# Kernel tuning notes

Measured on AMD Instinct MI355X. Metric: run time of the kernel, lower is better.

## Reference

```python
import jax, jax.numpy as jnp
import numpy as np

K = 3  # kernel_size
P = K // 2


def setup_inputs() -> dict:
    key = jax.random.key(0)
    k1, k2 = jax.random.split(key)
    x = jax.random.normal(k1, (8, 64, 256, 256), dtype=jnp.float32)
    alpha = jnp.full((1, 64, 1, 1), 0.1, dtype=jnp.float32)
    return {"x": x, "alpha": alpha}


def reference(x, alpha):
    # Equivalent to F.unfold(x, K, padding=P) -> abs-diff from center -> sum over K*K -> residual.
    b, c, h, w = x.shape
    xp = jnp.pad(x, ((0, 0), (0, 0), (P, P), (P, P)))  # zero padding, same as F.unfold
    diff_sum = jnp.zeros_like(x)
    for di in range(K):
        for dj in range(K):
            neighbor = xp[:, :, di:di + h, dj:dj + w]
            diff_sum = diff_sum + jnp.abs(x - neighbor)
    return x + alpha * diff_sum
```

## Files before the change

kernel.cpp:

```cpp
#include <hip/hip_runtime.h>


constexpr int H = 256;
constexpr int W = 256;
constexpr int C = 64;

__global__ __launch_bounds__(256) void adc_kernel(
    const float* __restrict__ x,
    const float* __restrict__ alpha,
    float* __restrict__ out)
{
    const int lane = threadIdx.x & 63;
    const int wave = threadIdx.x >> 6;
    const long slab = (long)blockIdx.x;
    const long img  = slab >> 4;
    const int  s16  = (int)(slab & 15);
    const int  y0   = s16 * 16 + wave * 4;
    const int  c    = (int)(img & (C - 1));

    const float  a    = alpha[c];
    const float* imgp = x   + img * (long)(H * W);
    float*       outp = out + img * (long)(H * W);
    const int    w0   = lane * 4;

    float v[6][6];
#pragma unroll
    for (int r = 0; r < 6; ++r) {
        const int yy = y0 + r - 1;
        float4 ctr = make_float4(0.f, 0.f, 0.f, 0.f);
        if (yy >= 0 && yy < H)
            ctr = *(const float4*)(imgp + (long)yy * W + w0);
        v[r][1] = ctr.x; v[r][2] = ctr.y; v[r][3] = ctr.z; v[r][4] = ctr.w;
        const float left  = __shfl_up(ctr.w, 1);
        const float right = __shfl_down(ctr.x, 1);
        v[r][0] = (lane == 0)  ? 0.f : left;
        v[r][5] = (lane == 63) ? 0.f : right;
    }

#pragma unroll
    for (int o = 0; o < 4; ++o) {
        float4 res;
        float* rp = &res.x;
#pragma unroll
        for (int j = 0; j < 4; ++j) {
            const float xc = v[o + 1][j + 1];
            float s = 0.f;
#pragma unroll
            for (int r = 0; r < 3; ++r)
#pragma unroll
                for (int d = 0; d < 3; ++d)
                    s += fabsf(xc - v[o + r][j + d]);
            rp[j] = fmaf(a, s, xc);
        }
        *(float4*)(outp + (long)(y0 + o) * W + w0) = res;
    }
}

extern "C" void kernel_launch(void* const* d_in, const int* in_sizes, int n_in,
                              void* d_out, int out_size, void* d_ws, size_t ws_size,
                              hipStream_t stream)
{
    const float* x     = (const float*)d_in[0];
    const float* alpha = (const float*)d_in[1];
    float*       out   = (float*)d_out;

    const int grid = 8 * C * (H / 16);
    adc_kernel<<<grid, 256, 0, stream>>>(x, alpha, out);
}
```

Before: 235.1 us.

## Stage slab rows in LDS via direct global-to-LDS loads, remap blocks per XCD

Each block now loads its 18-row halo slab straight into shared memory with global_load_lds and a zero-padded stride, instead of having every wave load six rows with shuffles. Adjacent waves no longer re-read the same halo rows from global memory. Stencil rows are then read from LDS in a rolling three-row window. Block indices are remapped so that all slabs of an image run on the same XCD, and outputs use nontemporal stores. In exchange the kernel adds a barrier and LDS traffic, and the global_load_lds path depends on the lane-to-address layout being correct.

```diff
diff --git a/kernel.cpp b/kernel.cpp
--- a/kernel.cpp
+++ b/kernel.cpp
@@ -1,58 +1,107 @@
 #include <hip/hip_runtime.h>
+#include <stdint.h>
 
+
+typedef float f32x4 __attribute__((ext_vector_type(4)));
 
 constexpr int H = 256;
 constexpr int W = 256;
 constexpr int C = 64;
+constexpr int SLAB = 16;
+constexpr int NR   = SLAB + 2;
+constexpr int RSTR = 264;
+
+typedef const uint32_t __attribute__((address_space(1)))* gas_t;
+typedef uint32_t __attribute__((address_space(3)))* las_t;
 
 __global__ __launch_bounds__(256) void adc_kernel(
     const float* __restrict__ x,
     const float* __restrict__ alpha,
     float* __restrict__ out)
 {
-    const int lane = threadIdx.x & 63;
-    const int wave = threadIdx.x >> 6;
-    const long slab = (long)blockIdx.x;
-    const long img  = slab >> 4;
-    const int  s16  = (int)(slab & 15);
-    const int  y0   = s16 * 16 + wave * 4;
-    const int  c    = (int)(img & (C - 1));
+    __shared__ float lds[NR * RSTR];
 
-    const float  a    = alpha[c];
-    const float* imgp = x   + img * (long)(H * W);
-    float*       outp = out + img * (long)(H * W);
-    const int    w0   = lane * 4;
+    const int tid  = threadIdx.x;
+    const int lane = tid & 63;
+    const int wave = tid >> 6;
 
-    float v[6][6];
-#pragma unroll
-    for (int r = 0; r < 6; ++r) {
-        const int yy = y0 + r - 1;
-        float4 ctr = make_float4(0.f, 0.f, 0.f, 0.f);
-        if (yy >= 0 && yy < H)
-            ctr = *(const float4*)(imgp + (long)yy * W + w0);
-        v[r][1] = ctr.x; v[r][2] = ctr.y; v[r][3] = ctr.z; v[r][4] = ctr.w;
-        const float left  = __shfl_up(ctr.w, 1);
-        const float right = __shfl_down(ctr.x, 1);
-        v[r][0] = (lane == 0)  ? 0.f : left;
-        v[r][5] = (lane == 63) ? 0.f : right;
+    const int n     = blockIdx.x;
+    const int xcd   = n & 7;
+    const int local = n >> 3;
+    const int img   = ((local >> 4) << 3) + xcd;
+    const int slab  = local & 15;
+    const int y0    = slab * SLAB;
+
+    const float a = alpha[img & (C - 1)];
+    const float* imgp = x   + (long)img * (H * W);
+    float*       outp = out + (long)img * (H * W);
+
+    if (tid < NR) {
+        *(f32x4*)&lds[tid * RSTR] = (f32x4){0.f, 0.f, 0.f, 0.f};
+        lds[tid * RSTR + 260] = 0.f;
     }
 
 #pragma unroll
+    for (int r = wave; r < NR; r += 4) {
+        const int g = y0 + r - 1;
+        if (g >= 0 && g < H) {
+            const float* gsrc = imgp + (long)g * W + lane * 4;
+            __builtin_amdgcn_global_load_lds((gas_t)gsrc,
+                                             (las_t)&lds[r * RSTR + 4],
+                                             16, 0, 0);
+        } else {
+            *(f32x4*)&lds[r * RSTR + 4 + lane * 4] =
+                (f32x4){0.f, 0.f, 0.f, 0.f};
+        }
+    }
+    __syncthreads();
+
+    const int r0    = wave * 4 + 1;
+    const int cbase = 4 + lane * 4;
+
+    f32x4 eq[3];
+    float eL[3], eR[3];
+#pragma unroll
+    for (int k = 0; k < 2; ++k) {
+        const int rr = r0 - 1 + k;
+        eq[k] = *(const f32x4*)&lds[rr * RSTR + cbase];
+        eL[k] = lds[rr * RSTR + cbase - 1];
+        eR[k] = lds[rr * RSTR + cbase + 4];
+    }
+
+    float* orow0 = outp + (long)(y0 + wave * 4) * W + lane * 4;
+
+#pragma unroll
     for (int o = 0; o < 4; ++o) {
-        float4 res;
-        float* rp = &res.x;
+        const int s = (o + 2) % 3, t = o % 3, m = (o + 1) % 3;
+        const int rr = r0 + o + 1;
+        eq[s] = *(const f32x4*)&lds[rr * RSTR + cbase];
+        eL[s] = lds[rr * RSTR + cbase - 1];
+        eR[s] = lds[rr * RSTR + cbase + 4];
+
+        float e[3][6];
+#pragma unroll
+        for (int k = 0; k < 3; ++k) {
+            const int kk = (k == 0) ? t : ((k == 1) ? m : s);
+            e[k][0] = eL[kk];
+            e[k][1] = eq[kk].x; e[k][2] = eq[kk].y;
+            e[k][3] = eq[kk].z; e[k][4] = eq[kk].w;
+            e[k][5] = eR[kk];
+        }
+
+        f32x4 res;
 #pragma unroll
         for (int j = 0; j < 4; ++j) {
-            const float xc = v[o + 1][j + 1];
-            float s = 0.f;
+            const float xc = e[1][j + 1];
+            float sacc = 0.f;
 #pragma unroll
-            for (int r = 0; r < 3; ++r)
+            for (int r2 = 0; r2 < 3; ++r2)
 #pragma unroll
                 for (int d = 0; d < 3; ++d)
-                    s += fabsf(xc - v[o + r][j + d]);
-            rp[j] = fmaf(a, s, xc);
+                    sacc += fabsf(xc - e[r2][j + d]);
+            res[j] = fmaf(a, sacc, xc);
         }
-        *(float4*)(outp + (long)(y0 + o) * W + w0) = res;
+        __builtin_nontemporal_store(res, (f32x4*)(orow0 + o * W));
     }
 }
 
@@ -64,6 +113,6 @@
     const float* alpha = (const float*)d_in[1];
     float*       out   = (float*)d_out;
 
-    const int grid = 8 * C * (H / 16);
+    const int grid = 8 * C * (H / SLAB);
     adc_kernel<<<grid, 256, 0, stream>>>(x, alpha, out);
 }
```

After: 228.1 us. 3.0% less time.

## Stream rows through per-wave LDS ring with async global-to-LDS loads

Applied to the files above, without the earlier changes.

Each wave now processes 16 rows instead of 4, streaming input rows through an 8-slot LDS ring filled by global_load_lds. Explicit vmcnt waits keep several loads in flight, and the three-row window is rotated in registers. This cuts halo re-reads from 6/4 to 18/16 and overlaps loads with compute. It also remaps blocks so each image's slabs stay on one XCD and uses nontemporal stores, at the cost of more LDS per block and fragile manual waitcnt tuning.

```diff
diff --git a/kernel.cpp b/kernel.cpp
--- a/kernel.cpp
+++ b/kernel.cpp
@@ -1,59 +1,102 @@
 #include <hip/hip_runtime.h>
+#include <stdint.h>
 
 
-constexpr int H = 256;
-constexpr int W = 256;
-constexpr int C = 64;
+typedef float f32x4 __attribute__((ext_vector_type(4)));
+
+constexpr int H = 256, W = 256, C = 64;
+constexpr int RSTR = 256;
+
+typedef const uint32_t __attribute__((address_space(1)))* gas_t;
+typedef uint32_t __attribute__((address_space(3)))* las_t;
+
+#define WAITV(n) do { asm volatile("s_waitcnt vmcnt(" #n ")" ::: "memory"); \
+                      __builtin_amdgcn_sched_barrier(0); } while (0)
 
 __global__ __launch_bounds__(256) void adc_kernel(
     const float* __restrict__ x,
     const float* __restrict__ alpha,
     float* __restrict__ out)
 {
-    const int lane = threadIdx.x & 63;
-    const int wave = threadIdx.x >> 6;
-    const long slab = (long)blockIdx.x;
-    const long img  = slab >> 4;
-    const int  s16  = (int)(slab & 15);
-    const int  y0   = s16 * 16 + wave * 4;
-    const int  c    = (int)(img & (C - 1));
+    __shared__ float lds[4 * 8 * RSTR];
 
-    const float  a    = alpha[c];
-    const float* imgp = x   + img * (long)(H * W);
-    float*       outp = out + img * (long)(H * W);
-    const int    w0   = lane * 4;
+    const int tid  = threadIdx.x, lane = tid & 63, wave = tid >> 6;
+    const int n    = blockIdx.x, xcd = n & 7, local = n >> 3;
+    const int img  = ((local >> 2) << 3) + xcd;
+    const int y0   = ((local & 3) * 4 + wave) * 16;
 
-    float v[6][6];
+    const float a = alpha[img & (C - 1)];
+    const float* imgp  = x   + (long)img * (H * W);
+    float*       outp  = out + (long)img * (H * W);
+    float*       wring = lds + wave * 8 * RSTR;
+
+    const f32x4 z4 = {0.f, 0.f, 0.f, 0.f};
+
 #pragma unroll
-    for (int r = 0; r < 6; ++r) {
-        const int yy = y0 + r - 1;
-        float4 ctr = make_float4(0.f, 0.f, 0.f, 0.f);
-        if (yy >= 0 && yy < H)
-            ctr = *(const float4*)(imgp + (long)yy * W + w0);
-        v[r][1] = ctr.x; v[r][2] = ctr.y; v[r][3] = ctr.z; v[r][4] = ctr.w;
-        const float left  = __shfl_up(ctr.w, 1);
-        const float right = __shfl_down(ctr.x, 1);
-        v[r][0] = (lane == 0)  ? 0.f : left;
-        v[r][5] = (lane == 63) ? 0.f : right;
+    for (int i = 0; i < 6; ++i) {
+        int g = y0 - 1 + i; if (g < 0) g = 0;
+        __builtin_amdgcn_global_load_lds(
+            (gas_t)(imgp + (long)g * W + lane * 4),
+            (las_t)&wring[(i & 7) * RSTR], 16, 0, 0);
     }
 
-#pragma unroll
-    for (int o = 0; o < 4; ++o) {
-        float4 res;
-        float* rp = &res.x;
-#pragma unroll
-        for (int j = 0; j < 4; ++j) {
-            const float xc = v[o + 1][j + 1];
-            float s = 0.f;
-#pragma unroll
-            for (int r = 0; r < 3; ++r)
-#pragma unroll
-                for (int d = 0; d < 3; ++d)
-                    s += fabsf(xc - v[o + r][j + d]);
-            rp[j] = fmaf(a, s, xc);
-        }
-        *(float4*)(outp + (long)(y0 + o) * W + w0) = res;
-    }
+    f32x4 m[3]; float eL[3], eR[3];
+
+#define READROW(I, K) {                                                  \
+        f32x4 f = *(const f32x4*)&wring[((I) & 7) * RSTR + lane * 4];    \
+        const float lft = __shfl_up(f.w, 1);                             \
+        const float rgt = __shfl_down(f.x, 1);                           \
+        m[K]  = f;                                                       \
+        eL[K] = (lane == 0)  ? 0.f : lft;           \
+        eR[K] = (lane == 63) ? 0.f : rgt; }
+
+#define ITER(O, WN_) {                                                   \
+        if ((O) < 12) {    \
+            const int i_ = (O) + 6;                                      \
+            int g_ = y0 + i_ - 1; if (g_ > H - 1) g_ = H - 1;            \
+            __builtin_amdgcn_global_load_lds(                            \
+                (gas_t)(imgp + (long)g_ * W + lane * 4),                 \
+                (las_t)&wring[(i_ & 7) * RSTR], 16, 0, 0);               \
+        }                                                                \
+        WAITV(WN_);            \
+        if ((O) == 0 && y0 == 0)                  \
+            *(f32x4*)&wring[0 * RSTR + lane * 4] = z4;                   \
+        if ((O) == 15 && y0 + 16 >= H)        \
+            *(f32x4*)&wring[(17 & 7) * RSTR + lane * 4] = z4;            \
+        if ((O) == 0) { READROW(0, 0) READROW(1, 1) }                    \
+        READROW((O) + 2, ((O) + 2) % 3)                                  \
+        {                                                                \
+            const int t_ = (O) % 3, c_ = ((O)+1) % 3, b_ = ((O)+2) % 3;  \
+            float e[3][6];                                               \
+            e[0][0]=eL[t_]; e[0][1]=m[t_].x; e[0][2]=m[t_].y;            \
+            e[0][3]=m[t_].z; e[0][4]=m[t_].w; e[0][5]=eR[t_];            \
+            e[1][0]=eL[c_]; e[1][1]=m[c_].x; e[1][2]=m[c_].y;            \
+            e[1][3]=m[c_].z; e[1][4]=m[c_].w; e[1][5]=eR[c_];            \
+            e[2][0]=eL[b_]; e[2][1]=m[b_].x; e[2][2]=m[b_].y;            \
+            e[2][3]=m[b_].z; e[2][4]=m[b_].w; e[2][5]=eR[b_];            \
+            f32x4 res;                                                   \
+            _Pragma("unroll")                                            \
+            for (int j = 0; j < 4; ++j) {                                \
+                const float xc = e[1][j + 1];                            \
+                float s = 0.f;                                           \
+                _Pragma("unroll")                                        \
+                for (int r = 0; r < 3; ++r)                              \
+                    _Pragma("unroll")                                    \
+                    for (int d = 0; d < 3; ++d)                          \
+                        s += fabsf(xc - e[r][j + d]);  \
+                res[j] = fmaf(a, s, xc);                                 \
+            }                                                            \
+            __builtin_nontemporal_store(res,                             \
+                (f32x4*)(outp + (long)(y0 + (O)) * W + lane * 4));       \
+        } }
+
+    ITER(0, 4)  ITER(1, 5)  ITER(2, 6)  ITER(3, 7)
+    ITER(4, 8)  ITER(5, 8)  ITER(6, 8)  ITER(7, 8)
+    ITER(8, 8)  ITER(9, 8)  ITER(10, 8) ITER(11, 8)
+    ITER(12, 7) ITER(13, 6) ITER(14, 5) ITER(15, 4)
+
+#undef ITER
+#undef READROW
 }
 
 extern "C" void kernel_launch(void* const* d_in, const int* in_sizes, int n_in,
@@ -64,6 +107,6 @@
     const float* alpha = (const float*)d_in[1];
     float*       out   = (float*)d_out;
 
-    const int grid = 8 * C * (H / 16);
+    const int grid = 8 * C * 4;
     adc_kernel<<<grid, 256, 0, stream>>>(x, alpha, out);
 }
```

Result: no change. 231.4 us (-1.6%).
